# Kernel optimization log

Measured on AMD Instinct MI355X. Metric: run time of the kernel, lower is better.

Reference implementation:

```python
import jax, jax.numpy as jnp
import numpy as np

B = 131072
IN_DIM = 21   # velocity_dim * (past_frame + 2) = 3 * 7
HID = 512
OUT_DIM = 21  # 7 waypoints * 3 coords
SEG = 0.5     # segment width in in_same_segment
WW = 0.5      # rescale weight for same-segment elements
INVALID = -10000.0
VALID_THRESH = -5000.0


def setup_inputs() -> dict:
    key = jax.random.key(0)
    ks = jax.random.split(key, 9)
    velocities = jax.random.normal(ks[0], (B, IN_DIM), dtype=jnp.float32)
    gt = jax.random.normal(ks[1], (B, 7, 3), dtype=jnp.float32)
    # emulate warp_gt padding: some trailing waypoints are invalid sentinels
    pad_mask = jax.random.bernoulli(ks[2], 0.2, (B, 7, 1))
    gt = jnp.where(pad_mask, jnp.float32(INVALID), gt)
    s1 = 1.0 / np.sqrt(IN_DIM)
    s2 = 1.0 / np.sqrt(HID)
    W1 = jax.random.uniform(ks[3], (HID, IN_DIM), jnp.float32, -s1, s1)
    b1 = jax.random.uniform(ks[4], (HID,), jnp.float32, -s1, s1)
    W2 = jax.random.uniform(ks[5], (HID, HID), jnp.float32, -s2, s2)
    b2 = jax.random.uniform(ks[6], (HID,), jnp.float32, -s2, s2)
    W3 = jax.random.uniform(ks[7], (OUT_DIM, HID), jnp.float32, -s2, s2)
    b3 = jax.random.uniform(ks[8], (OUT_DIM,), jnp.float32, -s2, s2)
    return {"velocities": velocities, "gt": gt,
            "W1": W1, "b1": b1, "W2": W2, "b2": b2, "W3": W3, "b3": b3}


def reference(velocities, gt, W1, b1, W2, b2, W3, b3):
    # plan_head MLP: 21 -> 512 -> 512 -> 21
    h = jax.nn.relu(velocities @ W1.T + b1)
    h = jax.nn.relu(h @ W2.T + b2)
    out = h @ W3.T + b3                      # [B, 21]
    pred = out.reshape(-1, 7, 3)             # waypoints x1..x7, 3 coords each
    # segment-conditional weighted L1 loss (vectorized form of the Python loop)
    valid = gt > VALID_THRESH
    same_seg = jnp.floor(pred / SEG) == jnp.floor(gt / SEG)
    w = jnp.where(valid & same_seg, jnp.float32(WW), jnp.float32(1.0))
    diff = jnp.abs(pred * w - gt * w)
    num = jnp.sum(jnp.where(valid, diff, 0.0))
    den = jnp.sum(valid.astype(jnp.float32))
    return num / den
```

## Files before the change

### kernel.cpp

```cpp
#include <hip/hip_runtime.h>
#include <hip/hip_bf16.h>

typedef __bf16 bf16_t;
typedef __bf16 bf16x8 __attribute__((ext_vector_type(8)));
typedef float f32x4 __attribute__((ext_vector_type(4)));

#define IN_DIM 21
#define HID 512
#define OUT_DIM 21
#define M_TILE 64
#define LSTRIDE 520
#define THREADS 1024

__global__ void prep_kernel(const float* __restrict__ W1, const float* __restrict__ W2,
                            const float* __restrict__ W3,
                            bf16_t* __restrict__ W1f, bf16_t* __restrict__ W2f,
                            bf16_t* __restrict__ W3f) {
    int i = blockIdx.x * blockDim.x + threadIdx.x;
    int stride = gridDim.x * blockDim.x;
    const int NW2 = HID * HID;
    const int NW1 = 32 * 512;
    const int NW3 = 16 * 2 * 512;
    for (; i < NW2 + NW1 + NW3; i += stride) {
        if (i < NW2) {
            int j = i & 7, lane = (i >> 3) & 63, ntile = (i >> 9) & 31, kstep = i >> 14;
            int n = ntile * 16 + (lane & 15);
            int k = kstep * 32 + (lane >> 4) * 8 + j;
            W2f[i] = (bf16_t)W2[n * HID + k];
        } else if (i < NW2 + NW1) {
            int t = i - NW2;
            int j = t & 7, lane = (t >> 3) & 63, ntile = t >> 9;
            int n = ntile * 16 + (lane & 15);
            int k = (lane >> 4) * 8 + j;
            W1f[t] = (k < IN_DIM) ? (bf16_t)W1[n * IN_DIM + k] : (bf16_t)0.0f;
        } else {
            int t = i - NW2 - NW1;
            int j = t & 7, lane = (t >> 3) & 63, ot = (t >> 9) & 1, kstep = t >> 10;
            int o = ot * 16 + (lane & 15);
            int k = kstep * 32 + (lane >> 4) * 8 + j;
            W3f[t] = (o < OUT_DIM) ? (bf16_t)W3[o * HID + k] : (bf16_t)0.0f;
        }
    }
}

__global__ __launch_bounds__(THREADS)
void fused_kernel(const float* __restrict__ V, const float* __restrict__ gt,
                  const float* __restrict__ b1, const float* __restrict__ b2,
                  const float* __restrict__ b3,
                  const bf16_t* __restrict__ W1f, const bf16_t* __restrict__ W2f,
                  const bf16_t* __restrict__ W3f, float* __restrict__ accum) {
    __shared__ __align__(16) bf16_t vlds[M_TILE][32];
    __shared__ __align__(16) bf16_t h1[M_TILE][LSTRIDE];
    __shared__ __align__(16) bf16_t h2[M_TILE][LSTRIDE];
    __shared__ float redbuf[32];

    const int tid  = threadIdx.x;
    const int wave = tid >> 6;
    const int lane = tid & 63;
    const int quad = lane >> 4;
    const int l16  = lane & 15;
    const long row0 = (long)blockIdx.x * M_TILE;

    for (int idx = tid; idx < M_TILE * 32; idx += THREADS) {
        int r = idx >> 5, c = idx & 31;
        float v = (c < IN_DIM) ? V[(row0 + r) * IN_DIM + c] : 0.0f;
        vlds[r][c] = (bf16_t)v;
    }
    __syncthreads();

    {
        bf16x8 a[4];
        #pragma unroll
        for (int mt = 0; mt < 4; ++mt)
            a[mt] = *reinterpret_cast<const bf16x8*>(&vlds[mt * 16 + l16][quad * 8]);
        #pragma unroll
        for (int nt = 0; nt < 2; ++nt) {
            int ntile = wave * 2 + nt;
            int n = ntile * 16 + l16;
            bf16x8 b = *reinterpret_cast<const bf16x8*>(W1f + ntile * 512 + lane * 8);
            float bias = b1[n];
            #pragma unroll
            for (int mt = 0; mt < 4; ++mt) {
                f32x4 c = {0.0f, 0.0f, 0.0f, 0.0f};
                c = __builtin_amdgcn_mfma_f32_16x16x32_bf16(a[mt], b, c, 0, 0, 0);
                #pragma unroll
                for (int r = 0; r < 4; ++r) {
                    float v = c[r] + bias;
                    v = v > 0.0f ? v : 0.0f;
                    h1[mt * 16 + quad * 4 + r][n] = (bf16_t)v;
                }
            }
        }
    }
    __syncthreads();

    {
        f32x4 acc[4][2];
        #pragma unroll
        for (int mt = 0; mt < 4; ++mt)
            #pragma unroll
            for (int nt = 0; nt < 2; ++nt)
                acc[mt][nt] = (f32x4){0.0f, 0.0f, 0.0f, 0.0f};

        const bf16_t* w2p0 = W2f + (wave * 2 + 0) * 512 + lane * 8;
        const bf16_t* w2p1 = W2f + (wave * 2 + 1) * 512 + lane * 8;

        for (int ks = 0; ks < 16; ++ks) {
            bf16x8 b0 = *reinterpret_cast<const bf16x8*>(w2p0 + ks * 32 * 512);
            bf16x8 b1v = *reinterpret_cast<const bf16x8*>(w2p1 + ks * 32 * 512);
            bf16x8 a[4];
            #pragma unroll
            for (int mt = 0; mt < 4; ++mt)
                a[mt] = *reinterpret_cast<const bf16x8*>(&h1[mt * 16 + l16][ks * 32 + quad * 8]);
            #pragma unroll
            for (int mt = 0; mt < 4; ++mt) {
                acc[mt][0] = __builtin_amdgcn_mfma_f32_16x16x32_bf16(a[mt], b0, acc[mt][0], 0, 0, 0);
                acc[mt][1] = __builtin_amdgcn_mfma_f32_16x16x32_bf16(a[mt], b1v, acc[mt][1], 0, 0, 0);
            }
        }

        #pragma unroll
        for (int nt = 0; nt < 2; ++nt) {
            int n = wave * 32 + nt * 16 + l16;
            float bias = b2[n];
            #pragma unroll
            for (int mt = 0; mt < 4; ++mt) {
                #pragma unroll
                for (int r = 0; r < 4; ++r) {
                    float v = acc[mt][nt][r] + bias;
                    v = v > 0.0f ? v : 0.0f;
                    h2[mt * 16 + quad * 4 + r][n] = (bf16_t)v;
                }
            }
        }
    }
    __syncthreads();

    if (wave < 8) {
        const int mt = wave >> 1;
        const int ot = wave & 1;
        f32x4 acc3 = {0.0f, 0.0f, 0.0f, 0.0f};
        for (int ks = 0; ks < 16; ++ks) {
            bf16x8 a = *reinterpret_cast<const bf16x8*>(&h2[mt * 16 + l16][ks * 32 + quad * 8]);
            bf16x8 b = *reinterpret_cast<const bf16x8*>(W3f + (ks * 2 + ot) * 512 + lane * 8);
            acc3 = __builtin_amdgcn_mfma_f32_16x16x32_bf16(a, b, acc3, 0, 0, 0);
        }

        float num = 0.0f, den = 0.0f;
        int col = ot * 16 + l16;
        if (col < OUT_DIM) {
            float bias = b3[col];
            #pragma unroll
            for (int r = 0; r < 4; ++r) {
                long grow = row0 + mt * 16 + quad * 4 + r;
                float pred = acc3[r] + bias;
                float g = gt[grow * OUT_DIM + col];
                if (g > -5000.0f) {
                    float w = (floorf(pred * 2.0f) == floorf(g * 2.0f)) ? 0.5f : 1.0f;
                    num += fabsf(pred * w - g * w);
                    den += 1.0f;
                }
            }
        }
        #pragma unroll
        for (int off = 32; off > 0; off >>= 1) {
            num += __shfl_down(num, off);
            den += __shfl_down(den, off);
        }
        if (lane == 0) { redbuf[wave * 2] = num; redbuf[wave * 2 + 1] = den; }
    }
    __syncthreads();
    if (tid == 0) {
        float n8 = 0.0f, d8 = 0.0f;
        #pragma unroll
        for (int w = 0; w < 8; ++w) { n8 += redbuf[w * 2]; d8 += redbuf[w * 2 + 1]; }
        atomicAdd(accum, n8);
        atomicAdd(accum + 1, d8);
    }
}

__global__ void finalize_kernel(const float* __restrict__ accum, float* __restrict__ out) {
    if (threadIdx.x == 0) out[0] = accum[0] / accum[1];
}

extern "C" void kernel_launch(void* const* d_in, const int* in_sizes, int n_in,
                              void* d_out, int out_size, void* d_ws, size_t ws_size,
                              hipStream_t stream) {
    const float* V  = (const float*)d_in[0];
    const float* gt = (const float*)d_in[1];
    const float* W1 = (const float*)d_in[2];
    const float* b1 = (const float*)d_in[3];
    const float* W2 = (const float*)d_in[4];
    const float* b2 = (const float*)d_in[5];
    const float* W3 = (const float*)d_in[6];
    const float* b3 = (const float*)d_in[7];
    float* out = (float*)d_out;

    char* ws = (char*)d_ws;
    float* accum = (float*)ws;
    bf16_t* W2f = (bf16_t*)(ws + 16);
    bf16_t* W1f = (bf16_t*)(ws + 16 + 512 * 512 * 2);
    bf16_t* W3f = (bf16_t*)(ws + 16 + 512 * 512 * 2 + 32 * 512 * 2);

    int Brows = in_sizes[0] / IN_DIM;
    int grid = Brows / M_TILE;

    hipMemsetAsync(accum, 0, 2 * sizeof(float), stream);
    prep_kernel<<<576, 512, 0, stream>>>(W1, W2, W3, W1f, W2f, W3f);
    fused_kernel<<<grid, THREADS, 0, stream>>>(V, gt, b1, b2, b3, W1f, W2f, W3f, accum);
    finalize_kernel<<<1, 64, 0, stream>>>(accum, out);
}
```

Measured before the change: 194.2 us.

## Transpose MLP tiles to 512-thread blocks with single LDS buffer and fused finalize

Cuts the block to 8 waves, each computing a 64x64 tile (4x4 MFMAs) with weights as the A operand and activations as B. This raises register reuse of weight fragments and halves the waves per block. The two hidden buffers are merged into one reused LDS array, which lowers LDS use so more blocks can fit per CU. Hidden writes are now vectorized bf16x4 stores. The separate finalize kernel is replaced by a last-block ticket counter, at the cost of an extra barrier and higher register pressure from 64 accumulator floats.

```diff
diff --git a/kernel.cpp b/kernel.cpp
--- a/kernel.cpp
+++ b/kernel.cpp
@@ -3,6 +3,7 @@
 
 typedef __bf16 bf16_t;
 typedef __bf16 bf16x8 __attribute__((ext_vector_type(8)));
+typedef __bf16 bf16x4 __attribute__((ext_vector_type(4)));
 typedef float f32x4 __attribute__((ext_vector_type(4)));
 
 #define IN_DIM 21
@@ -10,7 +11,7 @@
 #define OUT_DIM 21
 #define M_TILE 64
 #define LSTRIDE 520
-#define THREADS 1024
+#define THREADS 512
 
 __global__ void prep_kernel(const float* __restrict__ W1, const float* __restrict__ W2,
                             const float* __restrict__ W3,
@@ -23,14 +24,14 @@
     const int NW3 = 16 * 2 * 512;
     for (; i < NW2 + NW1 + NW3; i += stride) {
         if (i < NW2) {
-            int j = i & 7, lane = (i >> 3) & 63, ntile = (i >> 9) & 31, kstep = i >> 14;
-            int n = ntile * 16 + (lane & 15);
+            int j = i & 7, lane = (i >> 3) & 63, ht = (i >> 9) & 31, kstep = i >> 14;
+            int n = ht * 16 + (lane & 15);
             int k = kstep * 32 + (lane >> 4) * 8 + j;
             W2f[i] = (bf16_t)W2[n * HID + k];
         } else if (i < NW2 + NW1) {
             int t = i - NW2;
-            int j = t & 7, lane = (t >> 3) & 63, ntile = t >> 9;
-            int n = ntile * 16 + (lane & 15);
+            int j = t & 7, lane = (t >> 3) & 63, ht = t >> 9;
+            int n = ht * 16 + (lane & 15);
             int k = (lane >> 4) * 8 + j;
             W1f[t] = (k < IN_DIM) ? (bf16_t)W1[n * IN_DIM + k] : (bf16_t)0.0f;
         } else {
@@ -43,16 +44,17 @@
     }
 }
 
-__global__ __launch_bounds__(THREADS)
+__global__ __launch_bounds__(THREADS, 4)
 void fused_kernel(const float* __restrict__ V, const float* __restrict__ gt,
                   const float* __restrict__ b1, const float* __restrict__ b2,
                   const float* __restrict__ b3,
                   const bf16_t* __restrict__ W1f, const bf16_t* __restrict__ W2f,
-                  const bf16_t* __restrict__ W3f, float* __restrict__ accum) {
+                  const bf16_t* __restrict__ W3f, float* __restrict__ accum,
+                  unsigned int* __restrict__ counter, float* __restrict__ out,
+                  int nblocks) {
     __shared__ __align__(16) bf16_t vlds[M_TILE][32];
-    __shared__ __align__(16) bf16_t h1[M_TILE][LSTRIDE];
-    __shared__ __align__(16) bf16_t h2[M_TILE][LSTRIDE];
-    __shared__ float redbuf[32];
+    __shared__ __align__(16) bf16_t h[M_TILE][LSTRIDE];
+    __shared__ float redbuf[16];
 
     const int tid  = threadIdx.x;
     const int wave = tid >> 6;
@@ -69,92 +71,87 @@
     __syncthreads();
 
     {
-        bf16x8 a[4];
-        #pragma unroll
-        for (int mt = 0; mt < 4; ++mt)
-            a[mt] = *reinterpret_cast<const bf16x8*>(&vlds[mt * 16 + l16][quad * 8]);
-        #pragma unroll
-        for (int nt = 0; nt < 2; ++nt) {
-            int ntile = wave * 2 + nt;
-            int n = ntile * 16 + l16;
-            bf16x8 b = *reinterpret_cast<const bf16x8*>(W1f + ntile * 512 + lane * 8);
-            float bias = b1[n];
+        bf16x8 bfrag[4];
+        #pragma unroll
+        for (int nt = 0; nt < 4; ++nt)
+            bfrag[nt] = *reinterpret_cast<const bf16x8*>(&vlds[nt * 16 + l16][quad * 8]);
+        #pragma unroll
+        for (int mt = 0; mt < 4; ++mt) {
+            bf16x8 a = *reinterpret_cast<const bf16x8*>(W1f + (wave * 4 + mt) * 512 + lane * 8);
+            f32x4 bias = *reinterpret_cast<const f32x4*>(b1 + wave * 64 + mt * 16 + quad * 4);
             #pragma unroll
-            for (int mt = 0; mt < 4; ++mt) {
+            for (int nt = 0; nt < 4; ++nt) {
                 f32x4 c = {0.0f, 0.0f, 0.0f, 0.0f};
-                c = __builtin_amdgcn_mfma_f32_16x16x32_bf16(a[mt], b, c, 0, 0, 0);
+                c = __builtin_amdgcn_mfma_f32_16x16x32_bf16(a, bfrag[nt], c, 0, 0, 0);
+                bf16x4 hv;
                 #pragma unroll
                 for (int r = 0; r < 4; ++r) {
-                    float v = c[r] + bias;
-                    v = v > 0.0f ? v : 0.0f;
-                    h1[mt * 16 + quad * 4 + r][n] = (bf16_t)v;
+                    float v = c[r] + bias[r];
+                    hv[r] = (bf16_t)(v > 0.0f ? v : 0.0f);
                 }
+                *reinterpret_cast<bf16x4*>(&h[nt * 16 + l16][wave * 64 + mt * 16 + quad * 4]) = hv;
             }
         }
     }
     __syncthreads();
 
+    f32x4 acc[4][4];
+    #pragma unroll
+    for (int mt = 0; mt < 4; ++mt)
+        #pragma unroll
+        for (int nt = 0; nt < 4; ++nt)
+            acc[mt][nt] = (f32x4){0.0f, 0.0f, 0.0f, 0.0f};
+
+    for (int ks = 0; ks < 16; ++ks) {
+        bf16x8 bfrag[4];
+        #pragma unroll
+        for (int nt = 0; nt < 4; ++nt)
+            bfrag[nt] = *reinterpret_cast<const bf16x8*>(&h[nt * 16 + l16][ks * 32 + quad * 8]);
+        #pragma unroll
+        for (int mt = 0; mt < 4; ++mt) {
+            bf16x8 a = *reinterpret_cast<const bf16x8*>(
+                W2f + ks * 16384 + (wave * 4 + mt) * 512 + lane * 8);
+            #pragma unroll
+            for (int nt = 0; nt < 4; ++nt)
+                acc[mt][nt] = __builtin_amdgcn_mfma_f32_16x16x32_bf16(a, bfrag[nt], acc[mt][nt], 0, 0, 0);
+        }
+    }
+    __syncthreads();
+
+    #pragma unroll
+    for (int mt = 0; mt < 4; ++mt) {
+        f32x4 bias = *reinterpret_cast<const f32x4*>(b2 + wave * 64 + mt * 16 + quad * 4);
+        #pragma unroll
+        for (int nt = 0; nt < 4; ++nt) {
+            bf16x4 hv;
+            #pragma unroll
+            for (int r = 0; r < 4; ++r) {
+                float v = acc[mt][nt][r] + bias[r];
+                hv[r] = (bf16_t)(v > 0.0f ? v : 0.0f);
+            }
+            *reinterpret_cast<bf16x4*>(&h[nt * 16 + l16][wave * 64 + mt * 16 + quad * 4]) = hv;
+        }
+    }
+    __syncthreads();
+
     {
-        f32x4 acc[4][2];
-        #pragma unroll
-        for (int mt = 0; mt < 4; ++mt)
-            #pragma unroll
-            for (int nt = 0; nt < 2; ++nt)
-                acc[mt][nt] = (f32x4){0.0f, 0.0f, 0.0f, 0.0f};
-
-        const bf16_t* w2p0 = W2f + (wave * 2 + 0) * 512 + lane * 8;
-        const bf16_t* w2p1 = W2f + (wave * 2 + 1) * 512 + lane * 8;
-
-        for (int ks = 0; ks < 16; ++ks) {
-            bf16x8 b0 = *reinterpret_cast<const bf16x8*>(w2p0 + ks * 32 * 512);
-            bf16x8 b1v = *reinterpret_cast<const bf16x8*>(w2p1 + ks * 32 * 512);
-            bf16x8 a[4];
-            #pragma unroll
-            for (int mt = 0; mt < 4; ++mt)
-                a[mt] = *reinterpret_cast<const bf16x8*>(&h1[mt * 16 + l16][ks * 32 + quad * 8]);
-            #pragma unroll
-            for (int mt = 0; mt < 4; ++mt) {
-                acc[mt][0] = __builtin_amdgcn_mfma_f32_16x16x32_bf16(a[mt], b0, acc[mt][0], 0, 0, 0);
-                acc[mt][1] = __builtin_amdgcn_mfma_f32_16x16x32_bf16(a[mt], b1v, acc[mt][1], 0, 0, 0);
-            }
-        }
-
-        #pragma unroll
-        for (int nt = 0; nt < 2; ++nt) {
-            int n = wave * 32 + nt * 16 + l16;
-            float bias = b2[n];
-            #pragma unroll
-            for (int mt = 0; mt < 4; ++mt) {
-                #pragma unroll
-                for (int r = 0; r < 4; ++r) {
-                    float v = acc[mt][nt][r] + bias;
-                    v = v > 0.0f ? v : 0.0f;
-                    h2[mt * 16 + quad * 4 + r][n] = (bf16_t)v;
-                }
-            }
-        }
-    }
-    __syncthreads();
-
-    if (wave < 8) {
-        const int mt = wave >> 1;
         const int ot = wave & 1;
+        const int nt = wave >> 1;
         f32x4 acc3 = {0.0f, 0.0f, 0.0f, 0.0f};
         for (int ks = 0; ks < 16; ++ks) {
-            bf16x8 a = *reinterpret_cast<const bf16x8*>(&h2[mt * 16 + l16][ks * 32 + quad * 8]);
-            bf16x8 b = *reinterpret_cast<const bf16x8*>(W3f + (ks * 2 + ot) * 512 + lane * 8);
+            bf16x8 a = *reinterpret_cast<const bf16x8*>(W3f + (ks * 2 + ot) * 512 + lane * 8);
+            bf16x8 b = *reinterpret_cast<const bf16x8*>(&h[nt * 16 + l16][ks * 32 + quad * 8]);
             acc3 = __builtin_amdgcn_mfma_f32_16x16x32_bf16(a, b, acc3, 0, 0, 0);
         }
 
         float num = 0.0f, den = 0.0f;
-        int col = ot * 16 + l16;
-        if (col < OUT_DIM) {
-            float bias = b3[col];
-            #pragma unroll
-            for (int r = 0; r < 4; ++r) {
-                long grow = row0 + mt * 16 + quad * 4 + r;
-                float pred = acc3[r] + bias;
-                float g = gt[grow * OUT_DIM + col];
+        long brow = row0 + nt * 16 + l16;
+        #pragma unroll
+        for (int r = 0; r < 4; ++r) {
+            int c = ot * 16 + quad * 4 + r;
+            if (c < OUT_DIM) {
+                float pred = acc3[r] + b3[c];
+                float g = gt[brow * OUT_DIM + c];
                 if (g > -5000.0f) {
                     float w = (floorf(pred * 2.0f) == floorf(g * 2.0f)) ? 0.5f : 1.0f;
                     num += fabsf(pred * w - g * w);
@@ -176,11 +173,14 @@
         for (int w = 0; w < 8; ++w) { n8 += redbuf[w * 2]; d8 += redbuf[w * 2 + 1]; }
         atomicAdd(accum, n8);
         atomicAdd(accum + 1, d8);
-    }
-}
-
-__global__ void finalize_kernel(const float* __restrict__ accum, float* __restrict__ out) {
-    if (threadIdx.x == 0) out[0] = accum[0] / accum[1];
+        __threadfence();
+        unsigned int ticket = atomicAdd(counter, 1u);
+        if (ticket == (unsigned int)(nblocks - 1)) {
+            float tn = atomicAdd(accum, 0.0f);
+            float td = atomicAdd(accum + 1, 0.0f);
+            out[0] = tn / td;
+        }
+    }
 }
 
 extern "C" void kernel_launch(void* const* d_in, const int* in_sizes, int n_in,
@@ -198,6 +198,7 @@
 
     char* ws = (char*)d_ws;
     float* accum = (float*)ws;
+    unsigned int* counter = (unsigned int*)(ws + 8);
     bf16_t* W2f = (bf16_t*)(ws + 16);
     bf16_t* W1f = (bf16_t*)(ws + 16 + 512 * 512 * 2);
     bf16_t* W3f = (bf16_t*)(ws + 16 + 512 * 512 * 2 + 32 * 512 * 2);
@@ -205,8 +206,8 @@
     int Brows = in_sizes[0] / IN_DIM;
     int grid = Brows / M_TILE;
 
-    hipMemsetAsync(accum, 0, 2 * sizeof(float), stream);
+    hipMemsetAsync(ws, 0, 16, stream);
     prep_kernel<<<576, 512, 0, stream>>>(W1, W2, W3, W1f, W2f, W3f);
-    fused_kernel<<<grid, THREADS, 0, stream>>>(V, gt, b1, b2, b3, W1f, W2f, W3f, accum);
-    finalize_kernel<<<1, 64, 0, stream>>>(accum, out);
+    fused_kernel<<<grid, THREADS, 0, stream>>>(V, gt, b1, b2, b3, W1f, W2f, W3f,
+                                               accum, counter, out, grid);
 }
```

Measured after the change: 262.6 us. 1.35x slower.
